# Performance work log

Measured on AMD Instinct MI355X. Metric: run time of the kernel, lower is better.

Reference implementation:

```python
import jax, jax.numpy as jnp
import numpy as np

ALL_WINDOW_SIZES = [1, 2, 4, 8, 16, 32]
ATTENTION_WINDOW = 32
T, D, N = 8192, 128, 4096
NW = len(ALL_WINDOW_SIZES)


def _layernorm(x, g, b, eps=1e-5):
    mu = x.mean(axis=-1, keepdims=True)
    var = ((x - mu) ** 2).mean(axis=-1, keepdims=True)
    return (x - mu) / jnp.sqrt(var + eps) * g + b


def setup_inputs() -> dict:
    key = jax.random.key(0)
    ks = jax.random.split(key, 16)
    s = 0.02
    return {
        "inputEmbeds": jax.random.normal(ks[0], (T, D), dtype=jnp.float32),
        # per-neuron weights stacked -> Linear(D, N)
        "neuronW": jax.random.normal(ks[1], (D, N), dtype=jnp.float32) * s,
        "neuronB": jnp.zeros((N,), dtype=jnp.float32),
        # tiny attention layer (single head, Q/K/V projections)
        "Wq": jax.random.normal(ks[2], (D, D), dtype=jnp.float32) * s,
        "bq": jnp.zeros((D,), dtype=jnp.float32),
        "Wk": jax.random.normal(ks[3], (D, D), dtype=jnp.float32) * s,
        "bk": jnp.zeros((D,), dtype=jnp.float32),
        "Wv": jax.random.normal(ks[4], (D, D), dtype=jnp.float32) * s,
        "bv": jnp.zeros((D,), dtype=jnp.float32),
        # attentionProjection = LayerNorm(D) -> Linear(D, N)
        "ln_g": jnp.ones((D,), dtype=jnp.float32),
        "ln_b": jnp.zeros((D,), dtype=jnp.float32),
        "projW": jax.random.normal(ks[5], (D, N), dtype=jnp.float32) * s,
        "projb": jnp.zeros((N,), dtype=jnp.float32),
        "windowWeighting": jnp.ones((NW,), dtype=jnp.float32),
        # combinationLayer: Linear(N*NW, N)
        "comboW": jax.random.normal(ks[6], (N * NW, N), dtype=jnp.float32) * 0.005,
        "combob": jnp.zeros((N,), dtype=jnp.float32),
    }


def _tiny_attn(x, Wq, bq, Wk, bk, Wv, bv):
    # x: [B, W, D] -> single-head self attention
    q = x @ Wq + bq
    k = x @ Wk + bk
    v = x @ Wv + bv
    scores = jnp.einsum("bqd,bkd->bqk", q, k) / jnp.sqrt(jnp.asarray(x.shape[-1], x.dtype))
    return jnp.einsum("bqk,bkd->bqd", jax.nn.softmax(scores, axis=-1), v)


def reference(inputEmbeds, neuronW, neuronB, Wq, bq, Wk, bk, Wv, bv,
              ln_g, ln_b, projW, projb, windowWeighting, comboW, combob):
    # all neurons over all tokens: [T, N], tanh activation, clamp to [-5, 5]
    acts = jnp.clip(jnp.tanh(inputEmbeds @ neuronW + neuronB), -5.0, 5.0)

    window_means = []
    for w in ALL_WINDOW_SIZES:
        if w == ATTENTION_WINDOW:
            xw = inputEmbeds[-w:][None]  # [1, w, D]
            attended = _tiny_attn(xw, Wq, bq, Wk, bk, Wv, bv)  # [1, w, D]
            attn_mean = attended.mean(axis=1)  # [1, D]
            proj = _layernorm(attn_mean, ln_g, ln_b) @ projW + projb  # [1, N]
            window_means.append(proj)
        else:
            window_means.append(acts[-w:].mean(axis=0, keepdims=True))  # [1, N]

    norm_w = (windowWeighting + 0.1) / (windowWeighting.sum() + 0.1)
    weighted = jnp.concatenate(
        [window_means[i] * norm_w[i] for i in range(NW)], axis=1)  # [1, N*NW]
    return weighted @ comboW + combob  # [1, N]
```

## Files before the change

kernel.cpp:

```cpp
#include <hip/hip_runtime.h>

#define T_TOK 8192
#define D_DIM 128
#define N_NEU 4096
#define RPC 48
#define NCHUNK 512
#define PLAIN_CHUNKS 256

typedef float f4_t __attribute__((ext_vector_type(4)));

struct SmemActs {
    float xs16[16][128];
    float wst[32][256];
};
struct SmemQkv {
    float xs[32][128];
    float w[128][128];
};
union SmemA {
    SmemActs a;
    SmemQkv q;
};

__global__ void acts_qkv_kernel(
    const float* __restrict__ x,
    const float* __restrict__ neuronW, const float* __restrict__ neuronB,
    const float* __restrict__ Wq, const float* __restrict__ bq,
    const float* __restrict__ Wk, const float* __restrict__ bk,
    const float* __restrict__ Wv, const float* __restrict__ bv,
    const float* __restrict__ ww,
    float* __restrict__ v,
    float* __restrict__ qkv)
{
    __shared__ SmemA sm;
    const int tid = threadIdx.x;
    const int bid = blockIdx.x;

    if (bid < 16) {
        const int n0 = bid * 256;
        const int n = n0 + tid;
        for (int idx = tid; idx < 16 * 128; idx += 256) {
            int t = idx >> 7, d = idx & 127;
            sm.a.xs16[t][d] = x[(size_t)(T_TOK - 16 + t) * D_DIM + d];
        }
        float acc[16];
        float bias = neuronB[n];
#pragma unroll
        for (int t = 0; t < 16; ++t) acc[t] = bias;
        const f4_t* W4 = reinterpret_cast<const f4_t*>(neuronW);
        f4_t* wst4 = reinterpret_cast<f4_t*>(&sm.a.wst[0][0]);
        for (int c = 0; c < 4; ++c) {
            const int d0 = c * 32;
            __syncthreads();
#pragma unroll
            for (int k = 0; k < 8; ++k) {
                int idx = tid + k * 256;
                int dd = idx >> 6, j4 = idx & 63;
                wst4[dd * 64 + j4] = W4[(size_t)(d0 + dd) * 1024 + (n0 >> 2) + j4];
            }
            __syncthreads();
#pragma unroll
            for (int dd = 0; dd < 32; ++dd) {
                float w = sm.a.wst[dd][tid];
#pragma unroll
                for (int t = 0; t < 16; ++t) acc[t] += sm.a.xs16[t][d0 + dd] * w;
            }
        }
#pragma unroll
        for (int t = 0; t < 16; ++t) acc[t] = tanhf(acc[t]);
        float denom = 0.1f;
#pragma unroll
        for (int i = 0; i < 6; ++i) denom += ww[i];
        const float inv = 1.f / denom;
        float s1 = acc[15];
        float s2 = s1 + acc[14];
        float s4 = s2 + acc[13] + acc[12];
        float s8 = s4 + acc[11] + acc[10] + acc[9] + acc[8];
        float s16 = s8 + acc[7] + acc[6] + acc[5] + acc[4] + acc[3] + acc[2] + acc[1] + acc[0];
        v[0 * N_NEU + n] = s1 * ((ww[0] + 0.1f) * inv);
        v[1 * N_NEU + n] = s2 * 0.5f * ((ww[1] + 0.1f) * inv);
        v[2 * N_NEU + n] = s4 * 0.25f * ((ww[2] + 0.1f) * inv);
        v[3 * N_NEU + n] = s8 * 0.125f * ((ww[3] + 0.1f) * inv);
        v[4 * N_NEU + n] = s16 * 0.0625f * ((ww[4] + 0.1f) * inv);
        return;
    }

    const int m = bid - 16;
    const float* Wm = (m == 0) ? Wq : ((m == 1) ? Wk : Wv);
    const float* bb = (m == 0) ? bq : ((m == 1) ? bk : bv);

    f4_t* xs4 = reinterpret_cast<f4_t*>(&sm.q.xs[0][0]);
    const f4_t* X4 = reinterpret_cast<const f4_t*>(x + (size_t)(T_TOK - 32) * D_DIM);
#pragma unroll
    for (int k = 0; k < 4; ++k) xs4[tid + k * 256] = X4[tid + k * 256];
    f4_t* w4 = reinterpret_cast<f4_t*>(&sm.q.w[0][0]);
    const f4_t* Wm4 = reinterpret_cast<const f4_t*>(Wm);
#pragma unroll
    for (int k = 0; k < 16; ++k) w4[tid + k * 256] = Wm4[tid + k * 256];
    __syncthreads();

    const int d = tid & 127;
    const int g = tid >> 7;
    float acc[16];
    float bias = bb[d];
#pragma unroll
    for (int i = 0; i < 16; ++i) acc[i] = bias;
#pragma unroll 4
    for (int e = 0; e < 128; ++e) {
        float w = sm.q.w[e][d];
#pragma unroll
        for (int i = 0; i < 16; ++i) acc[i] += sm.q.xs[g * 16 + i][e] * w;
    }
#pragma unroll
    for (int i = 0; i < 16; ++i) qkv[m * 4096 + (g * 16 + i) * 128 + d] = acc[i];
}

struct SmemAP {
    union {
        struct {
            float qs[32][128];
            float kt[128][33];
            float vs[32][128];
            float ps[32][33];
            float pbar[32];
            float mvec[128];
            float red[2];
        } a;
        struct {
            float wst[32][256];
        } p;
    } u;
    float ys[128];
};

__global__ void attn_proj_kernel(
    const float* __restrict__ qkv,
    const float* __restrict__ ln_g, const float* __restrict__ ln_b,
    const float* __restrict__ projW,
    const float* __restrict__ projb,
    const float* __restrict__ ww,
    float* __restrict__ v)
{
    __shared__ SmemAP sm;
    const int tid = threadIdx.x;

    for (int idx = tid; idx < 32 * 128; idx += 256) {
        int i = idx >> 7, d = idx & 127;
        sm.u.a.qs[i][d] = qkv[idx];
        sm.u.a.kt[d][i] = qkv[4096 + idx];
        sm.u.a.vs[i][d] = qkv[8192 + idx];
    }
    __syncthreads();
    const float scale = 0.08838834764831845f;
#pragma unroll
    for (int rep = 0; rep < 4; ++rep) {
        int idx = tid + rep * 256;
        int i = idx >> 5, j = idx & 31;
        float acc = 0.f;
        for (int e = 0; e < 128; ++e) acc += sm.u.a.qs[i][e] * sm.u.a.kt[e][j];
        sm.u.a.ps[i][j] = acc * scale;
    }
    __syncthreads();
    if (tid < 32) {
        float mx = -1e30f;
        for (int j = 0; j < 32; ++j) mx = fmaxf(mx, sm.u.a.ps[tid][j]);
        float s = 0.f;
        for (int j = 0; j < 32; ++j) { float e = expf(sm.u.a.ps[tid][j] - mx); sm.u.a.ps[tid][j] = e; s += e; }
        float inv = 1.f / s;
        for (int j = 0; j < 32; ++j) sm.u.a.ps[tid][j] *= inv;
    }
    __syncthreads();
    if (tid < 32) {
        float s = 0.f;
        for (int i = 0; i < 32; ++i) s += sm.u.a.ps[i][tid];
        sm.u.a.pbar[tid] = s * (1.f / 32.f);
    }
    __syncthreads();
    if (tid < 128) {
        float s = 0.f;
        for (int j = 0; j < 32; ++j) s += sm.u.a.pbar[j] * sm.u.a.vs[j][tid];
        sm.u.a.mvec[tid] = s;
    }
    __syncthreads();
    if (tid < 64) {
        float p = sm.u.a.mvec[tid] + sm.u.a.mvec[tid + 64];
        for (int off = 32; off; off >>= 1) p += __shfl_down(p, off);
        if (tid == 0) sm.u.a.red[0] = p * (1.f / 128.f);
    }
    __syncthreads();
    float mu = sm.u.a.red[0];
    if (tid < 64) {
        float t1 = sm.u.a.mvec[tid] - mu, t2 = sm.u.a.mvec[tid + 64] - mu;
        float p = t1 * t1 + t2 * t2;
        for (int off = 32; off; off >>= 1) p += __shfl_down(p, off);
        if (tid == 0) sm.u.a.red[1] = rsqrtf(p * (1.f / 128.f) + 1e-5f);
    }
    __syncthreads();
    if (tid < 128) {
        sm.ys[tid] = (sm.u.a.mvec[tid] - mu) * sm.u.a.red[1] * ln_g[tid] + ln_b[tid];
    }
    __syncthreads();

    const int n0 = blockIdx.x * 256;
    const int n = n0 + tid;
    float denom = 0.1f;
#pragma unroll
    for (int i = 0; i < 6; ++i) denom += ww[i];
    const float nw5 = (ww[5] + 0.1f) / denom;

    float acc = projb[n];
    const f4_t* P4 = reinterpret_cast<const f4_t*>(projW);
    f4_t* wst4 = reinterpret_cast<f4_t*>(&sm.u.p.wst[0][0]);
    for (int c = 0; c < 4; ++c) {
        const int d0 = c * 32;
        __syncthreads();
#pragma unroll
        for (int k = 0; k < 8; ++k) {
            int idx = tid + k * 256;
            int dd = idx >> 6, j4 = idx & 63;
            wst4[dd * 64 + j4] = P4[(size_t)(d0 + dd) * 1024 + (n0 >> 2) + j4];
        }
        __syncthreads();
#pragma unroll
        for (int dd = 0; dd < 32; ++dd) {
            acc += sm.ys[d0 + dd] * sm.u.p.wst[dd][tid];
        }
    }
    v[5 * N_NEU + n] = acc * nw5;
}

__global__ __launch_bounds__(256) void combo_partial_kernel(
    const float* __restrict__ v,
    const float* __restrict__ comboW,
    float* __restrict__ part)
{
    __shared__ float vsm[RPC];
    const int tid = threadIdx.x;
    const int chunk = blockIdx.x;
    const int row0 = chunk * RPC;

    if (tid < RPC) vsm[tid] = v[row0 + tid];
    __syncthreads();

    const f4_t* W4 = reinterpret_cast<const f4_t*>(comboW);
    const size_t base = (size_t)row0 * 1024 + tid;
    f4_t acc0 = {0.f,0.f,0.f,0.f}, acc1 = {0.f,0.f,0.f,0.f};
    f4_t acc2 = {0.f,0.f,0.f,0.f}, acc3 = {0.f,0.f,0.f,0.f};

    if (chunk < PLAIN_CHUNKS) {
#pragma unroll 4
        for (int r = 0; r < RPC; ++r) {
            const float vr = vsm[r];
            const size_t b = base + (size_t)r * 1024;
            f4_t w0 = W4[b];
            f4_t w1 = W4[b + 256];
            f4_t w2 = W4[b + 512];
            f4_t w3 = W4[b + 768];
            acc0 += w0 * vr; acc1 += w1 * vr; acc2 += w2 * vr; acc3 += w3 * vr;
        }
    } else {
#pragma unroll 4
        for (int r = 0; r < RPC; ++r) {
            const float vr = vsm[r];
            const size_t b = base + (size_t)r * 1024;
            f4_t w0 = __builtin_nontemporal_load(&W4[b]);
            f4_t w1 = __builtin_nontemporal_load(&W4[b + 256]);
            f4_t w2 = __builtin_nontemporal_load(&W4[b + 512]);
            f4_t w3 = __builtin_nontemporal_load(&W4[b + 768]);
            acc0 += w0 * vr; acc1 += w1 * vr; acc2 += w2 * vr; acc3 += w3 * vr;
        }
    }
    f4_t* P = reinterpret_cast<f4_t*>(part) + (size_t)chunk * 1024 + tid;
    P[0]   = acc0;
    P[256] = acc1;
    P[512] = acc2;
    P[768] = acc3;
}

__global__ void combo_reduce_kernel(const float* __restrict__ part,
                                    const float* __restrict__ bias,
                                    float* __restrict__ out)
{
    __shared__ f4_t red[8][32];
    const int tid = threadIdx.x;
    const int h = tid >> 5;
    const int j = tid & 31;
    const int n4 = blockIdx.x * 32 + j;
    const f4_t* P4 = reinterpret_cast<const f4_t*>(part);
    f4_t acc = {0.f,0.f,0.f,0.f};
#pragma unroll 8
    for (int c = h * 64; c < h * 64 + 64; ++c)
        acc += P4[(size_t)c * 1024 + n4];
    red[h][j] = acc;
    __syncthreads();
    if (h == 0) {
        f4_t s = red[0][j] + red[1][j] + red[2][j] + red[3][j]
               + red[4][j] + red[5][j] + red[6][j] + red[7][j];
        s += reinterpret_cast<const f4_t*>(bias)[n4];
        reinterpret_cast<f4_t*>(out)[n4] = s;
    }
}

extern "C" void kernel_launch(void* const* d_in, const int* in_sizes, int n_in,
                              void* d_out, int out_size, void* d_ws, size_t ws_size,
                              hipStream_t stream) {
    const float* inputEmbeds = (const float*)d_in[0];
    const float* neuronW     = (const float*)d_in[1];
    const float* neuronB     = (const float*)d_in[2];
    const float* Wq          = (const float*)d_in[3];
    const float* bq          = (const float*)d_in[4];
    const float* Wk          = (const float*)d_in[5];
    const float* bk          = (const float*)d_in[6];
    const float* Wv          = (const float*)d_in[7];
    const float* bv          = (const float*)d_in[8];
    const float* ln_g        = (const float*)d_in[9];
    const float* ln_b        = (const float*)d_in[10];
    const float* projW       = (const float*)d_in[11];
    const float* projb       = (const float*)d_in[12];
    const float* ww          = (const float*)d_in[13];
    const float* comboW      = (const float*)d_in[14];
    const float* combob      = (const float*)d_in[15];
    float* out = (float*)d_out;
    float* ws  = (float*)d_ws;

    float* v    = ws;
    float* qkv  = ws + 24576;
    float* part = ws + 36864;

    acts_qkv_kernel<<<19, 256, 0, stream>>>(inputEmbeds, neuronW, neuronB,
                                            Wq, bq, Wk, bk, Wv, bv, ww, v, qkv);
    attn_proj_kernel<<<16, 256, 0, stream>>>(qkv, ln_g, ln_b, projW, projb, ww, v);
    combo_partial_kernel<<<NCHUNK, 256, 0, stream>>>(v, comboW, part);
    combo_reduce_kernel<<<32, 256, 0, stream>>>(part, combob, out);
}
```

Before: 107.8 us.

## Fuse QKV projection, attention and output projection into single front kernel

Result: slower. 131.8 us (+22.2%).

```diff
diff --git a/kernel.cpp b/kernel.cpp
--- a/kernel.cpp
+++ b/kernel.cpp
@@ -13,28 +13,44 @@
     float xs16[16][128];
     float wst[32][256];
 };
-struct SmemQkv {
+struct SmemChain {
     float xs[32][128];
-    float w[128][128];
+    union {
+        float w[128][128];
+        float pw[32][256];
+    } wu;
+    float qs[32][128];
+    float kt[128][33];
+    float ps[32][33];
+    float pbar[32];
+    float mvec[128];
+    float red[2];
+    float ys[128];
 };
 union SmemA {
     SmemActs a;
-    SmemQkv q;
+    SmemChain c;
 };
 
-__global__ void acts_qkv_kernel(
+__global__ void front_kernel(
     const float* __restrict__ x,
     const float* __restrict__ neuronW, const float* __restrict__ neuronB,
     const float* __restrict__ Wq, const float* __restrict__ bq,
     const float* __restrict__ Wk, const float* __restrict__ bk,
     const float* __restrict__ Wv, const float* __restrict__ bv,
+    const float* __restrict__ ln_g, const float* __restrict__ ln_b,
+    const float* __restrict__ projW, const float* __restrict__ projb,
     const float* __restrict__ ww,
-    float* __restrict__ v,
-    float* __restrict__ qkv)
+    float* __restrict__ v)
 {
     __shared__ SmemA sm;
     const int tid = threadIdx.x;
     const int bid = blockIdx.x;
+
+    float denom = 0.1f;
+#pragma unroll
+    for (int i = 0; i < 6; ++i) denom += ww[i];
+    const float winv = 1.f / denom;
 
     if (bid < 16) {
         const int n0 = bid * 256;
@@ -68,149 +84,143 @@
         }
 #pragma unroll
         for (int t = 0; t < 16; ++t) acc[t] = tanhf(acc[t]);
-        float denom = 0.1f;
-#pragma unroll
-        for (int i = 0; i < 6; ++i) denom += ww[i];
-        const float inv = 1.f / denom;
         float s1 = acc[15];
         float s2 = s1 + acc[14];
         float s4 = s2 + acc[13] + acc[12];
         float s8 = s4 + acc[11] + acc[10] + acc[9] + acc[8];
         float s16 = s8 + acc[7] + acc[6] + acc[5] + acc[4] + acc[3] + acc[2] + acc[1] + acc[0];
-        v[0 * N_NEU + n] = s1 * ((ww[0] + 0.1f) * inv);
-        v[1 * N_NEU + n] = s2 * 0.5f * ((ww[1] + 0.1f) * inv);
-        v[2 * N_NEU + n] = s4 * 0.25f * ((ww[2] + 0.1f) * inv);
-        v[3 * N_NEU + n] = s8 * 0.125f * ((ww[3] + 0.1f) * inv);
-        v[4 * N_NEU + n] = s16 * 0.0625f * ((ww[4] + 0.1f) * inv);
+        v[0 * N_NEU + n] = s1 * ((ww[0] + 0.1f) * winv);
+        v[1 * N_NEU + n] = s2 * 0.5f * ((ww[1] + 0.1f) * winv);
+        v[2 * N_NEU + n] = s4 * 0.25f * ((ww[2] + 0.1f) * winv);
+        v[3 * N_NEU + n] = s8 * 0.125f * ((ww[3] + 0.1f) * winv);
+        v[4 * N_NEU + n] = s16 * 0.0625f * ((ww[4] + 0.1f) * winv);
         return;
     }
-
-    const int m = bid - 16;
-    const float* Wm = (m == 0) ? Wq : ((m == 1) ? Wk : Wv);
-    const float* bb = (m == 0) ? bq : ((m == 1) ? bk : bv);
-
-    f4_t* xs4 = reinterpret_cast<f4_t*>(&sm.q.xs[0][0]);
-    const f4_t* X4 = reinterpret_cast<const f4_t*>(x + (size_t)(T_TOK - 32) * D_DIM);
-#pragma unroll
-    for (int k = 0; k < 4; ++k) xs4[tid + k * 256] = X4[tid + k * 256];
-    f4_t* w4 = reinterpret_cast<f4_t*>(&sm.q.w[0][0]);
-    const f4_t* Wm4 = reinterpret_cast<const f4_t*>(Wm);
-#pragma unroll
-    for (int k = 0; k < 16; ++k) w4[tid + k * 256] = Wm4[tid + k * 256];
-    __syncthreads();
 
     const int d = tid & 127;
     const int g = tid >> 7;
-    float acc[16];
-    float bias = bb[d];
-#pragma unroll
-    for (int i = 0; i < 16; ++i) acc[i] = bias;
-#pragma unroll 4
-    for (int e = 0; e < 128; ++e) {
-        float w = sm.q.w[e][d];
-#pragma unroll
-        for (int i = 0; i < 16; ++i) acc[i] += sm.q.xs[g * 16 + i][e] * w;
-    }
-#pragma unroll
-    for (int i = 0; i < 16; ++i) qkv[m * 4096 + (g * 16 + i) * 128 + d] = acc[i];
-}
-
-struct SmemAP {
-    union {
-        struct {
-            float qs[32][128];
-            float kt[128][33];
-            float vs[32][128];
-            float ps[32][33];
-            float pbar[32];
-            float mvec[128];
-            float red[2];
-        } a;
-        struct {
-            float wst[32][256];
-        } p;
-    } u;
-    float ys[128];
-};
-
-__global__ void attn_proj_kernel(
-    const float* __restrict__ qkv,
-    const float* __restrict__ ln_g, const float* __restrict__ ln_b,
-    const float* __restrict__ projW,
-    const float* __restrict__ projb,
-    const float* __restrict__ ww,
-    float* __restrict__ v)
-{
-    __shared__ SmemAP sm;
-    const int tid = threadIdx.x;
-
-    for (int idx = tid; idx < 32 * 128; idx += 256) {
-        int i = idx >> 7, d = idx & 127;
-        sm.u.a.qs[i][d] = qkv[idx];
-        sm.u.a.kt[d][i] = qkv[4096 + idx];
-        sm.u.a.vs[i][d] = qkv[8192 + idx];
-    }
-    __syncthreads();
+
+    f4_t* xs4 = reinterpret_cast<f4_t*>(&sm.c.xs[0][0]);
+    const f4_t* X4 = reinterpret_cast<const f4_t*>(x + (size_t)(T_TOK - 32) * D_DIM);
+#pragma unroll
+    for (int k = 0; k < 4; ++k) xs4[tid + k * 256] = X4[tid + k * 256];
+
+    f4_t* w4 = reinterpret_cast<f4_t*>(&sm.c.wu.w[0][0]);
+    float vacc[16];
+    {
+        const f4_t* Wm4 = reinterpret_cast<const f4_t*>(Wq);
+#pragma unroll
+        for (int k = 0; k < 16; ++k) w4[tid + k * 256] = Wm4[tid + k * 256];
+        __syncthreads();
+        float acc[16];
+        float bias = bq[d];
+#pragma unroll
+        for (int i = 0; i < 16; ++i) acc[i] = bias;
+#pragma unroll 4
+        for (int e = 0; e < 128; ++e) {
+            float w = sm.c.wu.w[e][d];
+#pragma unroll
+            for (int i = 0; i < 16; ++i) acc[i] += sm.c.xs[g * 16 + i][e] * w;
+        }
+#pragma unroll
+        for (int i = 0; i < 16; ++i) sm.c.qs[g * 16 + i][d] = acc[i];
+    }
+    __syncthreads();
+    {
+        const f4_t* Wm4 = reinterpret_cast<const f4_t*>(Wk);
+#pragma unroll
+        for (int k = 0; k < 16; ++k) w4[tid + k * 256] = Wm4[tid + k * 256];
+        __syncthreads();
+        float acc[16];
+        float bias = bk[d];
+#pragma unroll
+        for (int i = 0; i < 16; ++i) acc[i] = bias;
+#pragma unroll 4
+        for (int e = 0; e < 128; ++e) {
+            float w = sm.c.wu.w[e][d];
+#pragma unroll
+            for (int i = 0; i < 16; ++i) acc[i] += sm.c.xs[g * 16 + i][e] * w;
+        }
+#pragma unroll
+        for (int i = 0; i < 16; ++i) sm.c.kt[d][g * 16 + i] = acc[i];
+    }
+    __syncthreads();
+    {
+        const f4_t* Wm4 = reinterpret_cast<const f4_t*>(Wv);
+#pragma unroll
+        for (int k = 0; k < 16; ++k) w4[tid + k * 256] = Wm4[tid + k * 256];
+        __syncthreads();
+        float bias = bv[d];
+#pragma unroll
+        for (int i = 0; i < 16; ++i) vacc[i] = bias;
+#pragma unroll 4
+        for (int e = 0; e < 128; ++e) {
+            float w = sm.c.wu.w[e][d];
+#pragma unroll
+            for (int i = 0; i < 16; ++i) vacc[i] += sm.c.xs[g * 16 + i][e] * w;
+        }
+    }
+    __syncthreads();
+#pragma unroll
+    for (int i = 0; i < 16; ++i) sm.c.xs[g * 16 + i][d] = vacc[i];
+    __syncthreads();
+
     const float scale = 0.08838834764831845f;
 #pragma unroll
     for (int rep = 0; rep < 4; ++rep) {
         int idx = tid + rep * 256;
         int i = idx >> 5, j = idx & 31;
         float acc = 0.f;
-        for (int e = 0; e < 128; ++e) acc += sm.u.a.qs[i][e] * sm.u.a.kt[e][j];
-        sm.u.a.ps[i][j] = acc * scale;
+        for (int e = 0; e < 128; ++e) acc += sm.c.qs[i][e] * sm.c.kt[e][j];
+        sm.c.ps[i][j] = acc * scale;
     }
     __syncthreads();
     if (tid < 32) {
         float mx = -1e30f;
-        for (int j = 0; j < 32; ++j) mx = fmaxf(mx, sm.u.a.ps[tid][j]);
+        for (int j = 0; j < 32; ++j) mx = fmaxf(mx, sm.c.ps[tid][j]);
         float s = 0.f;
-        for (int j = 0; j < 32; ++j) { float e = expf(sm.u.a.ps[tid][j] - mx); sm.u.a.ps[tid][j] = e; s += e; }
+        for (int j = 0; j < 32; ++j) { float e = expf(sm.c.ps[tid][j] - mx); sm.c.ps[tid][j] = e; s += e; }
         float inv = 1.f / s;
-        for (int j = 0; j < 32; ++j) sm.u.a.ps[tid][j] *= inv;
+        for (int j = 0; j < 32; ++j) sm.c.ps[tid][j] *= inv;
     }
     __syncthreads();
     if (tid < 32) {
         float s = 0.f;
-        for (int i = 0; i < 32; ++i) s += sm.u.a.ps[i][tid];
-        sm.u.a.pbar[tid] = s * (1.f / 32.f);
+        for (int i = 0; i < 32; ++i) s += sm.c.ps[i][tid];
+        sm.c.pbar[tid] = s * (1.f / 32.f);
     }
     __syncthreads();
     if (tid < 128) {
         float s = 0.f;
-        for (int j = 0; j < 32; ++j) s += sm.u.a.pbar[j] * sm.u.a.vs[j][tid];
-        sm.u.a.mvec[tid] = s;
+        for (int j = 0; j < 32; ++j) s += sm.c.pbar[j] * sm.c.xs[j][tid];
+        sm.c.mvec[tid] = s;
     }
     __syncthreads();
     if (tid < 64) {
-        float p = sm.u.a.mvec[tid] + sm.u.a.mvec[tid + 64];
+        float p = sm.c.mvec[tid] + sm.c.mvec[tid + 64];
         for (int off = 32; off; off >>= 1) p += __shfl_down(p, off);
-        if (tid == 0) sm.u.a.red[0] = p * (1.f / 128.f);
-    }
-    __syncthreads();
-    float mu = sm.u.a.red[0];
+        if (tid == 0) sm.c.red[0] = p * (1.f / 128.f);
+    }
+    __syncthreads();
+    float mu = sm.c.red[0];
     if (tid < 64) {
-        float t1 = sm.u.a.mvec[tid] - mu, t2 = sm.u.a.mvec[tid + 64] - mu;
+        float t1 = sm.c.mvec[tid] - mu, t2 = sm.c.mvec[tid + 64] - mu;
         float p = t1 * t1 + t2 * t2;
         for (int off = 32; off; off >>= 1) p += __shfl_down(p, off);
-        if (tid == 0) sm.u.a.red[1] = rsqrtf(p * (1.f / 128.f) + 1e-5f);
+        if (tid == 0) sm.c.red[1] = rsqrtf(p * (1.f / 128.f) + 1e-5f);
     }
     __syncthreads();
     if (tid < 128) {
-        sm.ys[tid] = (sm.u.a.mvec[tid] - mu) * sm.u.a.red[1] * ln_g[tid] + ln_b[tid];
-    }
-    __syncthreads();
-
-    const int n0 = blockIdx.x * 256;
+        sm.c.ys[tid] = (sm.c.mvec[tid] - mu) * sm.c.red[1] * ln_g[tid] + ln_b[tid];
+    }
+    __syncthreads();
+
+    const int n0 = (bid - 16) * 256;
     const int n = n0 + tid;
-    float denom = 0.1f;
-#pragma unroll
-    for (int i = 0; i < 6; ++i) denom += ww[i];
-    const float nw5 = (ww[5] + 0.1f) / denom;
-
+    const float nw5 = (ww[5] + 0.1f) * winv;
     float acc = projb[n];
     const f4_t* P4 = reinterpret_cast<const f4_t*>(projW);
-    f4_t* wst4 = reinterpret_cast<f4_t*>(&sm.u.p.wst[0][0]);
+    f4_t* pw4 = reinterpret_cast<f4_t*>(&sm.c.wu.pw[0][0]);
     for (int c = 0; c < 4; ++c) {
         const int d0 = c * 32;
         __syncthreads();
@@ -218,12 +228,12 @@
         for (int k = 0; k < 8; ++k) {
             int idx = tid + k * 256;
             int dd = idx >> 6, j4 = idx & 63;
-            wst4[dd * 64 + j4] = P4[(size_t)(d0 + dd) * 1024 + (n0 >> 2) + j4];
+            pw4[dd * 64 + j4] = P4[(size_t)(d0 + dd) * 1024 + (n0 >> 2) + j4];
         }
         __syncthreads();
 #pragma unroll
         for (int dd = 0; dd < 32; ++dd) {
-            acc += sm.ys[d0 + dd] * sm.u.p.wst[dd][tid];
+            acc += sm.c.ys[d0 + dd] * sm.c.wu.pw[dd][tid];
         }
     }
     v[5 * N_NEU + n] = acc * nw5;
@@ -324,12 +334,11 @@
     float* ws  = (float*)d_ws;
 
     float* v    = ws;
-    float* qkv  = ws + 24576;
-    float* part = ws + 36864;
-
-    acts_qkv_kernel<<<19, 256, 0, stream>>>(inputEmbeds, neuronW, neuronB,
-                                            Wq, bq, Wk, bk, Wv, bv, ww, v, qkv);
-    attn_proj_kernel<<<16, 256, 0, stream>>>(qkv, ln_g, ln_b, projW, projb, ww, v);
+    float* part = ws + 24576;
+
+    front_kernel<<<32, 256, 0, stream>>>(inputEmbeds, neuronW, neuronB,
+                                         Wq, bq, Wk, bk, Wv, bv,
+                                         ln_g, ln_b, projW, projb, ww, v);
     combo_partial_kernel<<<NCHUNK, 256, 0, stream>>>(v, comboW, part);
     combo_reduce_kernel<<<32, 256, 0, stream>>>(part, combob, out);
 }
```
